# Kernel tuning notes

Hardware: AMD Instinct MI355X
Metric: run time of the kernel (lower is better)

The kernel has to match this reference:

```python
import jax, jax.numpy as jnp
import numpy as np

TEMPERATURE = 0.5
EPS = 1e-10

N, C, H, W = 8, 256, 96, 96
T, V = 32, 256
NUM_CLASSES = 19


def setup_inputs() -> dict:
    key = jax.random.key(0)
    k1, k2, k3, k4 = jax.random.split(key, 4)
    features = jax.random.normal(k1, (N, C, H, W), dtype=jnp.float32)
    batch_inds = jax.random.randint(k2, (T,), 0, N, dtype=jnp.int32)
    sample_inds = jax.random.randint(k3, (T, V), 0, H * W).astype(jnp.int64)
    labels = jax.random.randint(k4, (T,), 0, NUM_CLASSES, dtype=jnp.int32)
    return {"features": features, "batch_inds": batch_inds,
            "sample_inds": sample_inds, "labels": labels}


def reference(features, batch_inds, sample_inds, labels):
    n, c, h, w = features.shape
    t, v = sample_inds.shape
    # --- anchor sampling: gather V pixels per (image, class) pair ---
    f = features.reshape(n, c, h * w)            # (N, C, HW)
    g = f[batch_inds]                            # (T, C, HW)
    sampled = jnp.take_along_axis(g, sample_inds[:, None, :], axis=2)  # (T, C, V)
    # --- contrastive loss ---
    norm = jnp.maximum(jnp.linalg.norm(sampled, axis=1, keepdims=True), 1e-12)
    feats = sampled / norm                       # L2 normalize along C
    feats = jnp.swapaxes(feats, 1, 2).reshape(t * v, c)  # (T*V, C)
    lab = jnp.repeat(labels, v)                  # (T*V,)
    dot = (feats @ feats.T) / TEMPERATURE        # (T*V, T*V)
    eq = (lab[:, None] == lab[None, :]).astype(dot.dtype)
    diag = jnp.eye(t * v, dtype=dot.dtype)
    pos_mask = eq * (1.0 - diag)
    neg_mask = 1.0 - eq
    # stable SupCon loss: logsumexp over {self-exp + all negatives}
    logits = dot - jax.lax.stop_gradient(jnp.max(dot, axis=1, keepdims=True))
    exp_logits = jnp.exp(logits)
    neg_sum = jnp.sum(exp_logits * neg_mask, axis=1, keepdims=True)
    log_prob = logits - jnp.log(exp_logits + neg_sum)
    mean_log_prob_pos = jnp.sum(pos_mask * log_prob, axis=1) / jnp.maximum(
        jnp.sum(pos_mask, axis=1), EPS)
    return -jnp.mean(mean_log_prob_pos)
```

## Files before the change

### kernel.cpp

```cpp
#include <hip/hip_runtime.h>
#include <hip/hip_bf16.h>


namespace {

constexpr int kC = 256;
constexpr int kHW = 96 * 96;
constexpr int kT = 32;
constexpr int kV = 256;
constexpr int kM = kT * kV;

typedef __attribute__((ext_vector_type(8))) short short8;
typedef __attribute__((ext_vector_type(4))) float f32x4;

__device__ inline unsigned short f2bf(float x) {
  __hip_bfloat16 h = __float2bfloat16(x);
  return __builtin_bit_cast(unsigned short, h);
}
__device__ inline float bf2f(unsigned short u) {
  unsigned int v = ((unsigned int)u) << 16;
  return __builtin_bit_cast(float, v);
}
__device__ inline void load_lds16(const unsigned short* g, unsigned short* l) {
  __builtin_amdgcn_global_load_lds(
      (const __attribute__((address_space(1))) void*)g,
      (__attribute__((address_space(3))) void*)l, 16, 0, 0);
}

__device__ inline void stage_tile(const unsigned short* __restrict__ F,
                                  unsigned short* lds, int ct, int w,
                                  int lane) {
#pragma unroll
  for (int i = 0; i < 8; ++i) {
    const int n = w * 512 + i * 64 + lane;
    const int j = n >> 5;
    const int m = (lane & 31) ^ (j & 31);
    load_lds16(F + ((size_t)(ct * 64 + j) << 8) + m * 8,
               lds + (size_t)(w * 512 + i * 64) * 8);
  }
}

}

__global__ __launch_bounds__(256) void k_prep(
    const int* __restrict__ labels, float* __restrict__ ns,
    float* __restrict__ out, int out_size, int* __restrict__ nact,
    ushort2* __restrict__ list, float* __restrict__ cscale) {
  const int tid = (int)threadIdx.x;
  __shared__ int s_lab[kT];
  if (tid < kT) s_lab[tid] = labels[tid];
  if (tid == 0) *nact = 0;
  for (int i = tid; i < kM; i += 256) ns[i] = 0.f;
  for (int i = tid; i < out_size; i += 256) out[i] = 0.f;
  __syncthreads();
  if (tid < kT) {
    int m = 0;
    for (int u = 0; u < kT; ++u) m += (s_lab[u] == s_lab[tid]) ? 1 : 0;
    cscale[tid] = 1.f / ((float)(m * kV - 1) * (float)kM);
  }
  for (int p = tid; p < kT * kT; p += 256) {
    const int ti = p >> 5, tj = p & 31;
    if (s_lab[ti] == s_lab[tj]) {
      int base = atomicAdd(nact, 16);
#pragma unroll
      for (int a = 0; a < 4; ++a)
#pragma unroll
        for (int b = 0; b < 4; ++b) {
          ushort2 e;
          e.x = (unsigned short)(ti * 4 + a);
          e.y = (unsigned short)(tj * 4 + b);
          list[base + a * 4 + b] = e;
        }
    }
  }
}

__global__ __launch_bounds__(256) void k_gather(
    const float* __restrict__ feat, const int* __restrict__ binds,
    const int* __restrict__ sinds, unsigned short* __restrict__ FT) {
  const int b = (int)blockIdx.x;
  const int c = (int)blockIdx.y;
  __shared__ alignas(16) float row[kHW];
  __shared__ int s_match[kT + 1];
  if (threadIdx.x == 0) {
    int cnt = 0;
    for (int t = 0; t < kT; ++t)
      if (binds[t] == b) s_match[1 + cnt++] = t;
    s_match[0] = cnt;
  }
  __syncthreads();
  const int cnt = s_match[0];
  if (cnt == 0) return;
  const float4* src4 = (const float4*)(feat + ((size_t)b * kC + c) * kHW);
  for (int i = (int)threadIdx.x; i < kHW / 4; i += 256)
    ((float4*)row)[i] = src4[i];
  __syncthreads();
  unsigned short* dst = FT + (size_t)c * kM;
  for (int mi = 1; mi <= cnt; ++mi) {
    const int t = s_match[mi];
    const int p = sinds[t * kV + threadIdx.x];
    dst[t * kV + threadIdx.x] = f2bf(row[p]);
  }
}

__global__ __launch_bounds__(256) void k_norm(
    const unsigned short* __restrict__ FT, unsigned short* __restrict__ F) {
  constexpr int PAD = 40;
  const int v0 = (int)blockIdx.x * 32;
  __shared__ alignas(16) unsigned short tile[kC][PAD];
  __shared__ float part[8][32];
  __shared__ float s_inv[32];
  const int tid = (int)threadIdx.x;
  {
    const int p4 = tid & 3, cb = tid >> 2;
    for (int c = cb; c < kC; c += 64) {
      int4 d = *(const int4*)(FT + (size_t)c * kM + v0 + p4 * 8);
      *(int4*)&tile[c][p4 * 8] = d;
    }
  }
  __syncthreads();
  {
    const int v = tid & 31, oct = tid >> 5;
    float ss = 0.f;
    for (int c = oct * 32; c < oct * 32 + 32; ++c) {
      float x = bf2f(tile[c][v]);
      ss += x * x;
    }
    part[oct][v] = ss;
  }
  __syncthreads();
  if (tid < 32) {
    float ss = 0.f;
#pragma unroll
    for (int o = 0; o < 8; ++o) ss += part[o][tid];
    s_inv[tid] = 1.0f / fmaxf(sqrtf(ss), 1e-12f);
  }
  __syncthreads();
#pragma unroll
  for (int p = 0; p < 4; ++p) {
    const int chunk = p * 256 + tid;
    const int v = chunk >> 5, c0 = (chunk & 31) << 3;
    const float inv = s_inv[v];
    alignas(16) unsigned short o[8];
#pragma unroll
    for (int k = 0; k < 8; ++k) o[k] = f2bf(bf2f(tile[c0 + k][v]) * inv);
    *(int4*)(F + (size_t)(v0 + v) * kC + c0) = *(const int4*)o;
  }
}

__global__ __launch_bounds__(256, 2) void k_neg(
    const unsigned short* __restrict__ F, const int* __restrict__ labels,
    float* __restrict__ ns) {
  const int tid = (int)threadIdx.x;
  const int w = tid >> 6, lane = tid & 63, q = lane >> 4, l16 = lane & 15;
  const int wr = w >> 1, wc = w & 1;
  const int bid = (int)blockIdx.x;
  const int xcd = bid & 7, slot = bid >> 3;
  const int cx = xcd >> 1;
  const int row0 = (((slot << 1) | (xcd & 1))) * 64;
  __shared__ alignas(16) unsigned short Bt[2][64 * kC];
  __shared__ int s_lab[kT];
  __shared__ int s_tiles[32];
  __shared__ int s_nt;
  __shared__ float s_red[4][32];
  if (tid < kT) s_lab[tid] = labels[tid];
  __syncthreads();
  const int labr = s_lab[row0 >> 8];
  if (tid == 0) {
    int n = 0;
    for (int ct = cx * 32; ct < cx * 32 + 32; ++ct)
      if (s_lab[ct >> 2] != labr) s_tiles[n++] = ct;
    s_nt = n;
  }
  __syncthreads();
  const int nt = s_nt;
  if (nt == 0) return;

  stage_tile(F, Bt[0], row0 >> 6, w, lane);
  stage_tile(F, Bt[1], s_tiles[0], w, lane);
  __syncthreads();

  short8 af[2][8];
#pragma unroll
  for (int rg = 0; rg < 2; ++rg) {
    const int ja = wr * 32 + rg * 16 + l16;
    const unsigned short* arow = Bt[0] + ja * kC;
#pragma unroll
    for (int ks = 0; ks < 8; ++ks)
      af[rg][ks] = *(const short8*)(arow + (((ks * 4 + q) ^ (ja & 31)) << 3));
  }
  __syncthreads();

  const int jb0 = wc * 32 + l16, jb1 = wc * 32 + 16 + l16;
  const unsigned short* bc0base = (const unsigned short*)Bt + jb0 * kC;
  const unsigned short* bc1base = (const unsigned short*)Bt + jb1 * kC;
  int bofs0[8], bofs1[8];
#pragma unroll
  for (int ks = 0; ks < 8; ++ks) {
    bofs0[ks] = (((ks * 4 + q) ^ (jb0 & 31)) << 3);
    bofs1[ks] = (((ks * 4 + q) ^ (jb1 & 31)) << 3);
  }

  float sacc[2][4] = {};
  for (int it = 0; it < nt; ++it) {
    if (it + 1 < nt) stage_tile(F, Bt[it & 1], s_tiles[it + 1], w, lane);
    const size_t boff = (size_t)(1 ^ (it & 1)) * (64 * kC);
    const unsigned short* bc0 = bc0base + boff;
    const unsigned short* bc1 = bc1base + boff;
    f32x4 a00 = {0.f, 0.f, 0.f, 0.f}, a01 = a00, a10 = a00, a11 = a00;
#pragma unroll
    for (int ks = 0; ks < 8; ++ks) {
      short8 b0 = *(const short8*)(bc0 + bofs0[ks]);
      short8 b1 = *(const short8*)(bc1 + bofs1[ks]);
      a00 = __builtin_amdgcn_mfma_f32_16x16x32_bf16(af[0][ks], b0, a00, 0, 0, 0);
      a01 = __builtin_amdgcn_mfma_f32_16x16x32_bf16(af[0][ks], b1, a01, 0, 0, 0);
      a10 = __builtin_amdgcn_mfma_f32_16x16x32_bf16(af[1][ks], b0, a10, 0, 0, 0);
      a11 = __builtin_amdgcn_mfma_f32_16x16x32_bf16(af[1][ks], b1, a11, 0, 0, 0);
    }
#pragma unroll
    for (int r = 0; r < 4; ++r) {
      sacc[0][r] += __expf(fmaf(a00[r], 2.f, -2.f)) +
                    __expf(fmaf(a01[r], 2.f, -2.f));
      sacc[1][r] += __expf(fmaf(a10[r], 2.f, -2.f)) +
                    __expf(fmaf(a11[r], 2.f, -2.f));
    }
    __syncthreads();
  }

#pragma unroll
  for (int rg = 0; rg < 2; ++rg)
#pragma unroll
    for (int r = 0; r < 4; ++r) {
      float v = sacc[rg][r];
      v += __shfl_xor(v, 1, 64);
      v += __shfl_xor(v, 2, 64);
      v += __shfl_xor(v, 4, 64);
      v += __shfl_xor(v, 8, 64);
      if (l16 == 0) s_red[w][rg * 16 + q * 4 + r] = v;
    }
  __syncthreads();
  if (tid < 64) {
    const int rr = tid >> 5, e = tid & 31;
    float v = s_red[rr * 2][e] + s_red[rr * 2 + 1][e];
    atomicAdd(&ns[row0 + tid], v);
  }
}

__global__ __launch_bounds__(256, 3) void k_pos(
    const unsigned short* __restrict__ F, const float* __restrict__ ns,
    const int* __restrict__ nact, const ushort2* __restrict__ list,
    const float* __restrict__ cscale, float* __restrict__ out) {
  const int tid = (int)threadIdx.x;
  const int w = tid >> 6, lane = tid & 63, q = lane >> 4, l16 = lane & 15;
  const int wr = w >> 1, wc = w & 1;
  __shared__ alignas(16) unsigned short Bt[64 * kC];
  __shared__ float s_pos[4];
  const int n = *nact;

  const int jb0 = wc * 32 + l16, jb1 = wc * 32 + 16 + l16;
  int bofs0[8], bofs1[8];
#pragma unroll
  for (int ks = 0; ks < 8; ++ks) {
    bofs0[ks] = (((ks * 4 + q) ^ (jb0 & 31)) << 3);
    bofs1[ks] = (((ks * 4 + q) ^ (jb1 & 31)) << 3);
  }
  const unsigned short* bc0 = (const unsigned short*)Bt + jb0 * kC;
  const unsigned short* bc1 = (const unsigned short*)Bt + jb1 * kC;

  float pos = 0.f;
  for (int idx = (int)blockIdx.x; idx < n; idx += (int)gridDim.x) {
    const ushort2 e = list[idx];
    const int bi = e.x, bj = e.y;
    stage_tile(F, Bt, bj, w, lane);

    short8 af[2][8];
#pragma unroll
    for (int rg = 0; rg < 2; ++rg) {
      const int row = bi * 64 + wr * 32 + rg * 16 + l16;
#pragma unroll
      for (int ks = 0; ks < 8; ++ks)
        af[rg][ks] = *(const short8*)((const short*)F + (size_t)row * kC +
                                      ks * 32 + q * 8);
    }
    float nsv[2][4];
#pragma unroll
    for (int rg = 0; rg < 2; ++rg)
#pragma unroll
      for (int r = 0; r < 4; ++r)
        nsv[rg][r] = ns[bi * 64 + wr * 32 + rg * 16 + q * 4 + r];
    const float scale = cscale[bi >> 2];

    __syncthreads();

    f32x4 a00 = {0.f, 0.f, 0.f, 0.f}, a01 = a00, a10 = a00, a11 = a00;
#pragma unroll
    for (int ks = 0; ks < 8; ++ks) {
      short8 b0 = *(const short8*)(bc0 + bofs0[ks]);
      short8 b1 = *(const short8*)(bc1 + bofs1[ks]);
      a00 = __builtin_amdgcn_mfma_f32_16x16x32_bf16(af[0][ks], b0, a00, 0, 0, 0);
      a01 = __builtin_amdgcn_mfma_f32_16x16x32_bf16(af[0][ks], b1, a01, 0, 0, 0);
      a10 = __builtin_amdgcn_mfma_f32_16x16x32_bf16(af[1][ks], b0, a10, 0, 0, 0);
      a11 = __builtin_amdgcn_mfma_f32_16x16x32_bf16(af[1][ks], b1, a11, 0, 0, 0);
    }

    float tpos = 0.f;
#pragma unroll
    for (int rg = 0; rg < 2; ++rg)
#pragma unroll
      for (int cg = 0; cg < 2; ++cg) {
        const f32x4 acc = (rg == 0) ? (cg == 0 ? a00 : a01)
                                    : (cg == 0 ? a10 : a11);
        const int jc = bj * 64 + wc * 32 + cg * 16 + l16;
#pragma unroll
        for (int r = 0; r < 4; ++r) {
          const int i = bi * 64 + wr * 32 + rg * 16 + q * 4 + r;
          if (i != jc) {
            float d = fmaf(acc[r], 2.f, -2.f);
            tpos += d - __logf(__expf(d) + nsv[rg][r]);
          }
        }
      }
    pos += scale * tpos;
    __syncthreads();
  }

#pragma unroll
  for (int m = 1; m < 64; m <<= 1) pos += __shfl_xor(pos, m, 64);
  if (lane == 0) s_pos[w] = pos;
  __syncthreads();
  if (tid == 0)
    atomicAdd(out, -(s_pos[0] + s_pos[1] + s_pos[2] + s_pos[3]));
}

extern "C" void kernel_launch(void* const* d_in, const int* in_sizes, int n_in,
                              void* d_out, int out_size, void* d_ws,
                              size_t ws_size, hipStream_t stream) {
  const float* feat = (const float*)d_in[0];
  const int* binds = (const int*)d_in[1];
  const int* sinds = (const int*)d_in[2];
  const int* labels = (const int*)d_in[3];
  float* out = (float*)d_out;
  unsigned short* FT = (unsigned short*)d_ws;
  unsigned short* F = FT + (size_t)kC * kM;
  float* ns = (float*)(F + (size_t)kM * kC);
  int* nact = (int*)(ns + kM);
  float* cscale = (float*)(nact + 8);
  ushort2* list = (ushort2*)(cscale + 32);

  k_prep<<<1, 256, 0, stream>>>(labels, ns, out, out_size, nact, list, cscale);
  k_gather<<<dim3(8, kC), 256, 0, stream>>>(feat, binds, sinds, FT);
  k_norm<<<kM / 32, 256, 0, stream>>>(FT, F);
  k_neg<<<dim3(512), 256, 0, stream>>>(F, labels, ns);
  k_pos<<<768, 256, 0, stream>>>(F, ns, nact, list, cscale, out);
}
```

Before: 183.6 us.

## Widen k_neg to 128-row blocks with single-buffered B tile and parallelize ns zeroing

k_neg now runs 512-thread blocks covering 128 rows against a 16-column-tile panel, so each staged B tile feeds twice as many rows. The LDS double buffer becomes a single buffer with sync-stage-sync per tile, which lets more blocks fit per CU but gives up the overlap of loads with MFMA work. k_prep is launched with 64 blocks so zeroing ns is spread across the grid, and the tile staging helper is rewritten in flat thread-index form.

```diff
diff --git a/kernel.cpp b/kernel.cpp
--- a/kernel.cpp
+++ b/kernel.cpp
@@ -27,16 +27,27 @@
       (__attribute__((address_space(3))) void*)l, 16, 0, 0);
 }
 
-__device__ inline void stage_tile(const unsigned short* __restrict__ F,
-                                  unsigned short* lds, int ct, int w,
-                                  int lane) {
+__device__ inline void stage_tile4(const unsigned short* __restrict__ F,
+                                   unsigned short* lds, int ct, int tid) {
 #pragma unroll
   for (int i = 0; i < 8; ++i) {
-    const int n = w * 512 + i * 64 + lane;
+    const int n = i * 256 + tid;
     const int j = n >> 5;
-    const int m = (lane & 31) ^ (j & 31);
+    const int m = (n & 31) ^ (j & 31);
     load_lds16(F + ((size_t)(ct * 64 + j) << 8) + m * 8,
-               lds + (size_t)(w * 512 + i * 64) * 8);
+               lds + (size_t)n * 8);
+  }
+}
+
+__device__ inline void stage_tile8(const unsigned short* __restrict__ F,
+                                   unsigned short* lds, int ct, int tid) {
+#pragma unroll
+  for (int i = 0; i < 4; ++i) {
+    const int n = i * 512 + tid;
+    const int j = n >> 5;
+    const int m = (n & 31) ^ (j & 31);
+    load_lds16(F + ((size_t)(ct * 64 + j) << 8) + m * 8,
+               lds + (size_t)n * 8);
   }
 }
 
@@ -47,10 +58,12 @@
     float* __restrict__ out, int out_size, int* __restrict__ nact,
     ushort2* __restrict__ list, float* __restrict__ cscale) {
   const int tid = (int)threadIdx.x;
+  const int b = (int)blockIdx.x;
+  for (int i = b * 256 + tid; i < kM; i += 64 * 256) ns[i] = 0.f;
+  if (b != 0) return;
   __shared__ int s_lab[kT];
   if (tid < kT) s_lab[tid] = labels[tid];
   if (tid == 0) *nact = 0;
-  for (int i = tid; i < kM; i += 256) ns[i] = 0.f;
   for (int i = tid; i < out_size; i += 256) out[i] = 0.f;
   __syncthreads();
   if (tid < kT) {
@@ -65,11 +78,11 @@
 #pragma unroll
       for (int a = 0; a < 4; ++a)
 #pragma unroll
-        for (int b = 0; b < 4; ++b) {
+        for (int bb = 0; bb < 4; ++bb) {
           ushort2 e;
           e.x = (unsigned short)(ti * 4 + a);
-          e.y = (unsigned short)(tj * 4 + b);
-          list[base + a * 4 + b] = e;
+          e.y = (unsigned short)(tj * 4 + bb);
+          list[base + a * 4 + bb] = e;
         }
     }
   }
@@ -148,27 +161,27 @@
   }
 }
 
-__global__ __launch_bounds__(256, 2) void k_neg(
+__global__ __launch_bounds__(512, 4) void k_neg(
     const unsigned short* __restrict__ F, const int* __restrict__ labels,
     float* __restrict__ ns) {
   const int tid = (int)threadIdx.x;
   const int w = tid >> 6, lane = tid & 63, q = lane >> 4, l16 = lane & 15;
   const int wr = w >> 1, wc = w & 1;
   const int bid = (int)blockIdx.x;
-  const int xcd = bid & 7, slot = bid >> 3;
-  const int cx = xcd >> 1;
-  const int row0 = (((slot << 1) | (xcd & 1))) * 64;
-  __shared__ alignas(16) unsigned short Bt[2][64 * kC];
+  const int panel = bid & 7;
+  const int rb = bid >> 3;
+  const int row0 = rb * 128;
+  __shared__ alignas(16) unsigned short Bt[64 * kC];
   __shared__ int s_lab[kT];
-  __shared__ int s_tiles[32];
+  __shared__ int s_tiles[16];
   __shared__ int s_nt;
-  __shared__ float s_red[4][32];
+  __shared__ float s_red[8][32];
   if (tid < kT) s_lab[tid] = labels[tid];
   __syncthreads();
-  const int labr = s_lab[row0 >> 8];
+  const int labr = s_lab[rb >> 1];
   if (tid == 0) {
     int n = 0;
-    for (int ct = cx * 32; ct < cx * 32 + 32; ++ct)
+    for (int ct = panel * 16; ct < panel * 16 + 16; ++ct)
       if (s_lab[ct >> 2] != labr) s_tiles[n++] = ct;
     s_nt = n;
   }
@@ -176,42 +189,51 @@
   const int nt = s_nt;
   if (nt == 0) return;
 
-  stage_tile(F, Bt[0], row0 >> 6, w, lane);
-  stage_tile(F, Bt[1], s_tiles[0], w, lane);
-  __syncthreads();
-
   short8 af[2][8];
-#pragma unroll
-  for (int rg = 0; rg < 2; ++rg) {
-    const int ja = wr * 32 + rg * 16 + l16;
-    const unsigned short* arow = Bt[0] + ja * kC;
-#pragma unroll
-    for (int ks = 0; ks < 8; ++ks)
-      af[rg][ks] = *(const short8*)(arow + (((ks * 4 + q) ^ (ja & 31)) << 3));
-  }
-  __syncthreads();
-
-  const int jb0 = wc * 32 + l16, jb1 = wc * 32 + 16 + l16;
-  const unsigned short* bc0base = (const unsigned short*)Bt + jb0 * kC;
-  const unsigned short* bc1base = (const unsigned short*)Bt + jb1 * kC;
-  int bofs0[8], bofs1[8];
-#pragma unroll
-  for (int ks = 0; ks < 8; ++ks) {
-    bofs0[ks] = (((ks * 4 + q) ^ (jb0 & 31)) << 3);
-    bofs1[ks] = (((ks * 4 + q) ^ (jb1 & 31)) << 3);
-  }
+  stage_tile8(F, Bt, rb * 2, tid);
+  __syncthreads();
+  if (wr < 2) {
+#pragma unroll
+    for (int rg = 0; rg < 2; ++rg) {
+      const int ja = wr * 32 + rg * 16 + l16;
+      const unsigned short* arow = Bt + ja * kC;
+#pragma unroll
+      for (int ks = 0; ks < 8; ++ks)
+        af[rg][ks] =
+            *(const short8*)(arow + (((ks * 4 + q) ^ (ja & 31)) << 3));
+    }
+  }
+  __syncthreads();
+  stage_tile8(F, Bt, rb * 2 + 1, tid);
+  __syncthreads();
+  if (wr >= 2) {
+#pragma unroll
+    for (int rg = 0; rg < 2; ++rg) {
+      const int ja = (wr - 2) * 32 + rg * 16 + l16;
+      const unsigned short* arow = Bt + ja * kC;
+#pragma unroll
+      for (int ks = 0; ks < 8; ++ks)
+        af[rg][ks] =
+            *(const short8*)(arow + (((ks * 4 + q) ^ (ja & 31)) << 3));
+    }
+  }
+
+  const unsigned short* bc0 = Bt + (wc * 32 + l16) * kC;
+  const unsigned short* bc1 = bc0 + 16 * kC;
+  int bofs[8];
+#pragma unroll
+  for (int ks = 0; ks < 8; ++ks) bofs[ks] = ((ks * 4 + q) ^ l16) << 3;
 
   float sacc[2][4] = {};
   for (int it = 0; it < nt; ++it) {
-    if (it + 1 < nt) stage_tile(F, Bt[it & 1], s_tiles[it + 1], w, lane);
-    const size_t boff = (size_t)(1 ^ (it & 1)) * (64 * kC);
-    const unsigned short* bc0 = bc0base + boff;
-    const unsigned short* bc1 = bc1base + boff;
+    __syncthreads();
+    stage_tile8(F, Bt, s_tiles[it], tid);
+    __syncthreads();
     f32x4 a00 = {0.f, 0.f, 0.f, 0.f}, a01 = a00, a10 = a00, a11 = a00;
 #pragma unroll
     for (int ks = 0; ks < 8; ++ks) {
-      short8 b0 = *(const short8*)(bc0 + bofs0[ks]);
-      short8 b1 = *(const short8*)(bc1 + bofs1[ks]);
+      short8 b0 = *(const short8*)(bc0 + bofs[ks]);
+      short8 b1 = *(const short8*)(bc1 + (bofs[ks] ^ 128));
       a00 = __builtin_amdgcn_mfma_f32_16x16x32_bf16(af[0][ks], b0, a00, 0, 0, 0);
       a01 = __builtin_amdgcn_mfma_f32_16x16x32_bf16(af[0][ks], b1, a01, 0, 0, 0);
       a10 = __builtin_amdgcn_mfma_f32_16x16x32_bf16(af[1][ks], b0, a10, 0, 0, 0);
@@ -224,7 +246,6 @@
       sacc[1][r] += __expf(fmaf(a10[r], 2.f, -2.f)) +
                     __expf(fmaf(a11[r], 2.f, -2.f));
     }
-    __syncthreads();
   }
 
 #pragma unroll
@@ -239,7 +260,7 @@
       if (l16 == 0) s_red[w][rg * 16 + q * 4 + r] = v;
     }
   __syncthreads();
-  if (tid < 64) {
+  if (tid < 128) {
     const int rr = tid >> 5, e = tid & 31;
     float v = s_red[rr * 2][e] + s_red[rr * 2 + 1][e];
     atomicAdd(&ns[row0 + tid], v);
@@ -271,7 +292,7 @@
   for (int idx = (int)blockIdx.x; idx < n; idx += (int)gridDim.x) {
     const ushort2 e = list[idx];
     const int bi = e.x, bj = e.y;
-    stage_tile(F, Bt, bj, w, lane);
+    stage_tile4(F, Bt, bj, tid);
 
     short8 af[2][8];
 #pragma unroll
@@ -347,9 +368,9 @@
   float* cscale = (float*)(nact + 8);
   ushort2* list = (ushort2*)(cscale + 32);
 
-  k_prep<<<1, 256, 0, stream>>>(labels, ns, out, out_size, nact, list, cscale);
+  k_prep<<<64, 256, 0, stream>>>(labels, ns, out, out_size, nact, list, cscale);
   k_gather<<<dim3(8, kC), 256, 0, stream>>>(feat, binds, sinds, FT);
   k_norm<<<kM / 32, 256, 0, stream>>>(FT, F);
-  k_neg<<<dim3(512), 256, 0, stream>>>(F, labels, ns);
+  k_neg<<<dim3(512), 512, 0, stream>>>(F, labels, ns);
   k_pos<<<768, 256, 0, stream>>>(F, ns, nact, list, cscale, out);
 }
```

Result: faster. 178.5 us (-2.8%).
